# Kernel tuning notes

Measured on AMD Instinct MI355X. Metric: run time of the kernel, lower is better.

## Reference

```python
import jax, jax.numpy as jnp
import numpy as np

B, N, ENC, DEC, ATT = 32, 4096, 1024, 512, 512


def setup_inputs() -> dict:
    key = jax.random.key(0)
    ks = jax.random.split(key, 8)
    s_enc = 1.0 / np.sqrt(ENC)
    s_dec = 1.0 / np.sqrt(DEC)
    s_att = 1.0 / np.sqrt(ATT)
    return {
        "encoder_out": jax.random.normal(ks[0], (B, N, ENC), jnp.float32),
        "decoder_hidden": jax.random.normal(ks[1], (B, DEC), jnp.float32),
        "W_enc": jax.random.uniform(ks[2], (ENC, ATT), jnp.float32, -s_enc, s_enc),
        "b_enc": jax.random.uniform(ks[3], (ATT,), jnp.float32, -s_enc, s_enc),
        "W_dec": jax.random.uniform(ks[4], (DEC, ATT), jnp.float32, -s_dec, s_dec),
        "b_dec": jax.random.uniform(ks[5], (ATT,), jnp.float32, -s_dec, s_dec),
        "w_full": jax.random.uniform(ks[6], (ATT,), jnp.float32, -s_att, s_att),
        "b_full": jax.random.uniform(ks[7], (), jnp.float32, -s_att, s_att),
    }


def reference(encoder_out, decoder_hidden, W_enc, b_enc, W_dec, b_dec, w_full, b_full):
    # att1: [B, N, ATT]; att2: [B, 1, ATT]
    att1 = jnp.einsum('bne,ea->bna', encoder_out, W_enc) + b_enc
    att2 = (decoder_hidden @ W_dec + b_dec)[:, None, :]
    att = jax.nn.relu(att1 + att2)
    e = jnp.einsum('bna,a->bn', att, w_full) + b_full  # [B, N]
    alpha = jax.nn.softmax(e, axis=1)
    awe = jnp.einsum('bne,bn->be', encoder_out, alpha)  # weighted encoding [B, ENC]
    return awe, alpha
```

## Files before the change

### kernel.cpp

```cpp
#include <hip/hip_runtime.h>

#define B_ 32
#define N_ 4096
#define ENC_ 1024
#define DEC_ 512
#define ATT_ 512

typedef __attribute__((ext_vector_type(8))) short short8;
typedef __attribute__((ext_vector_type(4))) float f32x4;

__device__ __forceinline__ short f2bf(float f) {
  union { float f; unsigned u; } x; x.f = f;
  unsigned r = (x.u + 0x7FFFu + ((x.u >> 16) & 1u)) >> 16;
  return (short)r;
}

__device__ __forceinline__ void gl_lds16(const void* g, void* l) {
  __builtin_amdgcn_global_load_lds(
      (const __attribute__((address_space(1))) unsigned int*)g,
      (__attribute__((address_space(3))) unsigned int*)l, 16, 0, 0);
}

extern "C" __global__ void __launch_bounds__(256) prep_kernel(
    const float* __restrict__ dh, const float* __restrict__ W_dec,
    const float* __restrict__ b_dec, const float* __restrict__ b_enc,
    const float* __restrict__ W_enc,
    float* __restrict__ att2, short* __restrict__ Wfrag)
{
  if (blockIdx.x < B_) {
    __shared__ float dhs[DEC_];
    int b = blockIdx.x;
    for (int i = threadIdx.x; i < DEC_; i += 256) dhs[i] = dh[b * DEC_ + i];
    __syncthreads();
    for (int a = threadIdx.x; a < ATT_; a += 256) {
      float s = b_dec[a] + b_enc[a];
      for (int k = 0; k < DEC_; ++k) s += dhs[k] * W_dec[k * ATT_ + a];
      att2[b * ATT_ + a] = s;
    }
  } else {
    int idx = (blockIdx.x - B_) * 256 + threadIdx.x;
    int l = idx & 63;
    int t = (idx >> 6) & 31;
    int c = idx >> 11;
    int col = c * 16 + (l & 15);
    int kb = t * 32 + (l >> 4) * 8;
    short8 p;
#pragma unroll
    for (int j = 0; j < 8; ++j) p[j] = f2bf(W_enc[(kb + j) * ATT_ + col]);
    *(short8*)(Wfrag + ((long)idx << 3)) = p;
  }
}

extern "C" __global__ void __launch_bounds__(512, 2) gemm_e_kernel(
    const float* __restrict__ enc, const short* __restrict__ Wfrag,
    const float* __restrict__ att2, const float* __restrict__ w_full,
    float* __restrict__ e_out)
{
  __shared__ __align__(16) short As[2][128 * 32];
  __shared__ __align__(16) short Bs[2][32 * 512];
  __shared__ float e_red[2][64][4];

  const int tid = threadIdx.x;
  const int lane = tid & 63;
  const int w = tid >> 6;
  const int wr = w >> 2;
  const int wc = w & 3;
  const int blk = blockIdx.x;
  const int b = blk >> 5;
  const int n0 = (blk & 31) * 128;

  const int arow = tid >> 2;
  const int akc = tid & 3;
  const float* aptr = enc + ((long)(blk * 128 + arow)) * ENC_ + akc * 8;
  const int awbyte = (arow * 64 + akc * 16) ^ ((arow & 7) << 4);

  int arbyte[4];
#pragma unroll
  for (int r = 0; r < 4; ++r) {
    int rr = wr * 64 + r * 16 + (lane & 15);
    arbyte[r] = (rr * 64 + ((lane >> 4) * 16)) ^ ((rr & 7) << 4);
  }

  f32x4 acc[4][8] = {};

#pragma unroll
  for (int jj = 0; jj < 4; ++jj) {
    int c = (w << 2) + jj;
    gl_lds16(Wfrag + (((long)(c * 32 + 0) * 64 + lane) << 3), &Bs[0][c << 9]);
  }
  {
    f32x4 a0 = *(const f32x4*)(aptr);
    f32x4 a1 = *(const f32x4*)(aptr + 4);
    short8 p;
#pragma unroll
    for (int j = 0; j < 4; ++j) { p[j] = f2bf(a0[j]); p[j + 4] = f2bf(a1[j]); }
    *(short8*)((char*)(&As[0][0]) + awbyte) = p;
  }
  __syncthreads();

  for (int t = 0; t < 32; ++t) {
    const int cur = t & 1, nxt = cur ^ 1;
    f32x4 a0, a1;
    if (t < 31) {
#pragma unroll
      for (int jj = 0; jj < 4; ++jj) {
        int c = (w << 2) + jj;
        gl_lds16(Wfrag + (((long)(c * 32 + (t + 1)) * 64 + lane) << 3),
                 &Bs[nxt][c << 9]);
      }
      a0 = *(const f32x4*)(aptr + (t + 1) * 32);
      a1 = *(const f32x4*)(aptr + (t + 1) * 32 + 4);
    }

    short8 af[4];
#pragma unroll
    for (int r = 0; r < 4; ++r)
      af[r] = *(const short8*)((const char*)(&As[cur][0]) + arbyte[r]);
#pragma unroll
    for (int cc = 0; cc < 8; ++cc) {
      short8 bfg = *(const short8*)(&Bs[cur][((wc * 8 + cc) << 9) + (lane << 3)]);
#pragma unroll
      for (int r = 0; r < 4; ++r)
        acc[r][cc] = __builtin_amdgcn_mfma_f32_16x16x32_bf16(af[r], bfg,
                                                             acc[r][cc], 0, 0, 0);
    }

    if (t < 31) {
      short8 p;
#pragma unroll
      for (int j = 0; j < 4; ++j) { p[j] = f2bf(a0[j]); p[j + 4] = f2bf(a1[j]); }
      *(short8*)((char*)(&As[nxt][0]) + awbyte) = p;
    }
    __syncthreads();
  }

  const int lq = lane >> 4, lr = lane & 15;
  float at2v[8], wv[8];
#pragma unroll
  for (int cc = 0; cc < 8; ++cc) {
    int col = wc * 128 + cc * 16 + lr;
    at2v[cc] = att2[b * ATT_ + col];
    wv[cc] = w_full[col];
  }
#pragma unroll
  for (int r = 0; r < 4; ++r) {
#pragma unroll
    for (int j = 0; j < 4; ++j) {
      float s = 0.f;
#pragma unroll
      for (int cc = 0; cc < 8; ++cc)
        s += fmaxf(acc[r][cc][j] + at2v[cc], 0.f) * wv[cc];
      s += __shfl_xor(s, 1); s += __shfl_xor(s, 2);
      s += __shfl_xor(s, 4); s += __shfl_xor(s, 8);
      if (lr == 0) e_red[wr][r * 16 + lq * 4 + j][wc] = s;
    }
  }
  __syncthreads();
  if (tid < 128) {
    int wrr = tid >> 6, rl = tid & 63;
    float ev = e_red[wrr][rl][0] + e_red[wrr][rl][1] +
               e_red[wrr][rl][2] + e_red[wrr][rl][3];
    e_out[b * N_ + n0 + wrr * 64 + rl] = ev;
  }
}

extern "C" __global__ void __launch_bounds__(256) softmax_kernel(
    const float* __restrict__ e, float* __restrict__ alpha)
{
  int b = blockIdx.x, tid = threadIdx.x;
  float v[16];
  float m = -1e30f;
#pragma unroll
  for (int i = 0; i < 16; ++i) {
    v[i] = e[b * N_ + i * 256 + tid];
    m = fmaxf(m, v[i]);
  }
  for (int off = 1; off < 64; off <<= 1) m = fmaxf(m, __shfl_xor(m, off));
  __shared__ float redm[4];
  if ((tid & 63) == 0) redm[tid >> 6] = m;
  __syncthreads();
  m = fmaxf(fmaxf(redm[0], redm[1]), fmaxf(redm[2], redm[3]));
  float s = 0.f;
#pragma unroll
  for (int i = 0; i < 16; ++i) { v[i] = expf(v[i] - m); s += v[i]; }
  for (int off = 1; off < 64; off <<= 1) s += __shfl_xor(s, off);
  __shared__ float reds[4];
  if ((tid & 63) == 0) reds[tid >> 6] = s;
  __syncthreads();
  s = reds[0] + reds[1] + reds[2] + reds[3];
  float inv = 1.0f / s;
#pragma unroll
  for (int i = 0; i < 16; ++i) alpha[b * N_ + i * 256 + tid] = v[i] * inv;
}

extern "C" __global__ void __launch_bounds__(256) awe_part_kernel(
    const float* __restrict__ enc, const float* __restrict__ alpha,
    float* __restrict__ part)
{
  __shared__ float als[256];
  __shared__ f32x4 red[256];
  int bi = blockIdx.x;
  int b = bi & 31, cchunk = (bi >> 5) & 3, nchunk = bi >> 7;
  int t = threadIdx.x;
  int n0 = nchunk * 256;
  als[t] = alpha[b * N_ + n0 + t];
  __syncthreads();
  int tcol = t & 63, tn = t >> 6;
  const float* base = enc + (long)b * N_ * ENC_ + (long)n0 * ENC_ +
                      cchunk * 256 + tcol * 4;
  f32x4 acc = {};
  for (int i = tn; i < 256; i += 4) {
    f32x4 vv = *(const f32x4*)(base + (long)i * ENC_);
    acc += als[i] * vv;
  }
  red[t] = acc;
  __syncthreads();
  if (t < 64) {
    f32x4 s = red[t] + red[t + 64] + red[t + 128] + red[t + 192];
    *(f32x4*)(&part[(long)nchunk * 32768 + b * 1024 + cchunk * 256 + t * 4]) = s;
  }
}

extern "C" __global__ void __launch_bounds__(256) awe_reduce_kernel(
    const float* __restrict__ part, float* __restrict__ awe)
{
  int i = blockIdx.x * 256 + threadIdx.x;
  float s = 0.f;
#pragma unroll
  for (int p = 0; p < 16; ++p) s += part[(long)p * 32768 + i];
  awe[i] = s;
}

extern "C" void kernel_launch(void* const* d_in, const int* in_sizes, int n_in,
                              void* d_out, int out_size, void* d_ws, size_t ws_size,
                              hipStream_t stream) {
  const float* enc    = (const float*)d_in[0];
  const float* dh     = (const float*)d_in[1];
  const float* W_enc  = (const float*)d_in[2];
  const float* b_enc  = (const float*)d_in[3];
  const float* W_dec  = (const float*)d_in[4];
  const float* b_dec  = (const float*)d_in[5];
  const float* w_full = (const float*)d_in[6];
  float* out = (float*)d_out;

  char* ws = (char*)d_ws;
  float* att2  = (float*)ws;
  short* Wfrag = (short*)(ws + 65536);
  float* e_buf = (float*)(ws + 65536 + 1048576);
  float* part  = (float*)(ws + 65536 + 1048576 + 524288);

  hipLaunchKernelGGL(prep_kernel, dim3(B_ + 256), dim3(256), 0, stream,
                     dh, W_dec, b_dec, b_enc, W_enc, att2, Wfrag);
  hipLaunchKernelGGL(gemm_e_kernel, dim3(1024), dim3(512), 0, stream,
                     enc, Wfrag, att2, w_full, e_buf);
  hipLaunchKernelGGL(softmax_kernel, dim3(B_), dim3(256), 0, stream,
                     e_buf, out + B_ * ENC_);
  hipLaunchKernelGGL(awe_part_kernel, dim3(2048), dim3(256), 0, stream,
                     enc, out + B_ * ENC_, part);
  hipLaunchKernelGGL(awe_reduce_kernel, dim3(128), dim3(256), 0, stream,
                     part, out);
}
```

Before: 373.4 us.

## Shrink GEMM tile to 64 rows, load W fragments directly from global

The GEMM+score kernel moves from 128-row to 64-row tiles, doubling the grid to 2048 blocks. Each of the 8 waves now owns 64 attention columns and reads its bf16 W fragments straight from global/L2 into registers, so the large LDS buffer for B is dropped. LDS drops to a small double-buffered A tile, launch bounds allow 4 blocks per CU, and A prefetch now runs two steps ahead. The aim is higher occupancy and less LDS traffic, at the cost of more redundant W reads through L2 and per-iteration global-load latency on the MFMA path.

New measurement: 331.8 us. -11.1%, faster.

```diff
diff --git a/kernel.cpp b/kernel.cpp
--- a/kernel.cpp
+++ b/kernel.cpp
@@ -7,6 +7,7 @@
 #define ATT_ 512
 
 typedef __attribute__((ext_vector_type(8))) short short8;
+typedef __attribute__((ext_vector_type(4))) short short4v;
 typedef __attribute__((ext_vector_type(4))) float f32x4;
 
 __device__ __forceinline__ short f2bf(float f) {
@@ -15,10 +16,10 @@
   return (short)r;
 }
 
-__device__ __forceinline__ void gl_lds16(const void* g, void* l) {
-  __builtin_amdgcn_global_load_lds(
-      (const __attribute__((address_space(1))) unsigned int*)g,
-      (__attribute__((address_space(3))) unsigned int*)l, 16, 0, 0);
+__device__ __forceinline__ void lds_barrier() {
+  asm volatile("s_waitcnt lgkmcnt(0)" ::: "memory");
+  __builtin_amdgcn_s_barrier();
+  asm volatile("" ::: "memory");
 }
 
 extern "C" __global__ void __launch_bounds__(256) prep_kernel(
@@ -51,96 +52,87 @@
   }
 }
 
-extern "C" __global__ void __launch_bounds__(512, 2) gemm_e_kernel(
+extern "C" __global__ void __launch_bounds__(512, 4) gemm_e_kernel(
     const float* __restrict__ enc, const short* __restrict__ Wfrag,
     const float* __restrict__ att2, const float* __restrict__ w_full,
     float* __restrict__ e_out)
 {
-  __shared__ __align__(16) short As[2][128 * 32];
-  __shared__ __align__(16) short Bs[2][32 * 512];
-  __shared__ float e_red[2][64][4];
+  __shared__ __align__(16) short As[2][64 * 32];
+  __shared__ float e_red[64][8];
 
   const int tid = threadIdx.x;
   const int lane = tid & 63;
   const int w = tid >> 6;
-  const int wr = w >> 2;
-  const int wc = w & 3;
   const int blk = blockIdx.x;
-  const int b = blk >> 5;
-  const int n0 = (blk & 31) * 128;
-
-  const int arow = tid >> 2;
-  const int akc = tid & 3;
-  const float* aptr = enc + ((long)(blk * 128 + arow)) * ENC_ + akc * 8;
-  const int awbyte = (arow * 64 + akc * 16) ^ ((arow & 7) << 4);
+  const int b = blk >> 6;
+  const int n0 = (blk & 63) * 64;
+
+  const int arow = tid >> 3;
+  const int akc = tid & 7;
+  const float* aptr = enc + ((long)(b * N_ + n0 + arow)) * ENC_ + akc * 4;
+  const int awbyte = (arow * 64 + akc * 8) ^ ((arow & 7) << 4);
 
   int arbyte[4];
 #pragma unroll
   for (int r = 0; r < 4; ++r) {
-    int rr = wr * 64 + r * 16 + (lane & 15);
+    int rr = r * 16 + (lane & 15);
     arbyte[r] = (rr * 64 + ((lane >> 4) * 16)) ^ ((rr & 7) << 4);
   }
 
-  f32x4 acc[4][8] = {};
-
-#pragma unroll
-  for (int jj = 0; jj < 4; ++jj) {
-    int c = (w << 2) + jj;
-    gl_lds16(Wfrag + (((long)(c * 32 + 0) * 64 + lane) << 3), &Bs[0][c << 9]);
-  }
+  const short* bbase = Wfrag + (long)(w * 4) * 32 * 512 + lane * 8;
+
+  f32x4 acc[4][4] = {};
+
   {
-    f32x4 a0 = *(const f32x4*)(aptr);
-    f32x4 a1 = *(const f32x4*)(aptr + 4);
-    short8 p;
-#pragma unroll
-    for (int j = 0; j < 4; ++j) { p[j] = f2bf(a0[j]); p[j + 4] = f2bf(a1[j]); }
-    *(short8*)((char*)(&As[0][0]) + awbyte) = p;
-  }
-  __syncthreads();
-
+    f32x4 p0 = *(const f32x4*)(aptr);
+    short4v q;
+#pragma unroll
+    for (int j = 0; j < 4; ++j) q[j] = f2bf(p0[j]);
+    *(short4v*)((char*)(&As[0][0]) + awbyte) = q;
+  }
+  f32x4 pA = *(const f32x4*)(aptr + 32);
+  lds_barrier();
+
+#pragma unroll 2
   for (int t = 0; t < 32; ++t) {
-    const int cur = t & 1, nxt = cur ^ 1;
-    f32x4 a0, a1;
-    if (t < 31) {
-#pragma unroll
-      for (int jj = 0; jj < 4; ++jj) {
-        int c = (w << 2) + jj;
-        gl_lds16(Wfrag + (((long)(c * 32 + (t + 1)) * 64 + lane) << 3),
-                 &Bs[nxt][c << 9]);
-      }
-      a0 = *(const f32x4*)(aptr + (t + 1) * 32);
-      a1 = *(const f32x4*)(aptr + (t + 1) * 32 + 4);
-    }
+    const int cur = t & 1;
+    f32x4 pB;
+    if (t + 2 < 32) pB = *(const f32x4*)(aptr + (t + 2) * 32);
+
+    short8 bfg[4];
+#pragma unroll
+    for (int c = 0; c < 4; ++c)
+      bfg[c] = *(const short8*)(bbase + c * 16384 + t * 512);
 
     short8 af[4];
 #pragma unroll
     for (int r = 0; r < 4; ++r)
       af[r] = *(const short8*)((const char*)(&As[cur][0]) + arbyte[r]);
-#pragma unroll
-    for (int cc = 0; cc < 8; ++cc) {
-      short8 bfg = *(const short8*)(&Bs[cur][((wc * 8 + cc) << 9) + (lane << 3)]);
+
+#pragma unroll
+    for (int c = 0; c < 4; ++c)
 #pragma unroll
       for (int r = 0; r < 4; ++r)
-        acc[r][cc] = __builtin_amdgcn_mfma_f32_16x16x32_bf16(af[r], bfg,
-                                                             acc[r][cc], 0, 0, 0);
+        acc[r][c] = __builtin_amdgcn_mfma_f32_16x16x32_bf16(af[r], bfg[c],
+                                                            acc[r][c], 0, 0, 0);
+
+    if (t + 1 < 32) {
+      short4v q;
+#pragma unroll
+      for (int j = 0; j < 4; ++j) q[j] = f2bf(pA[j]);
+      *(short4v*)((char*)(&As[cur ^ 1][0]) + awbyte) = q;
     }
-
-    if (t < 31) {
-      short8 p;
-#pragma unroll
-      for (int j = 0; j < 4; ++j) { p[j] = f2bf(a0[j]); p[j + 4] = f2bf(a1[j]); }
-      *(short8*)((char*)(&As[nxt][0]) + awbyte) = p;
-    }
-    __syncthreads();
+    pA = pB;
+    lds_barrier();
   }
 
   const int lq = lane >> 4, lr = lane & 15;
-  float at2v[8], wv[8];
-#pragma unroll
-  for (int cc = 0; cc < 8; ++cc) {
-    int col = wc * 128 + cc * 16 + lr;
-    at2v[cc] = att2[b * ATT_ + col];
-    wv[cc] = w_full[col];
+  float at2v[4], wv[4];
+#pragma unroll
+  for (int c = 0; c < 4; ++c) {
+    int col = w * 64 + c * 16 + lr;
+    at2v[c] = att2[b * ATT_ + col];
+    wv[c] = w_full[col];
   }
 #pragma unroll
   for (int r = 0; r < 4; ++r) {
@@ -148,19 +140,19 @@
     for (int j = 0; j < 4; ++j) {
       float s = 0.f;
 #pragma unroll
-      for (int cc = 0; cc < 8; ++cc)
-        s += fmaxf(acc[r][cc][j] + at2v[cc], 0.f) * wv[cc];
+      for (int c = 0; c < 4; ++c)
+        s += fmaxf(acc[r][c][j] + at2v[c], 0.f) * wv[c];
       s += __shfl_xor(s, 1); s += __shfl_xor(s, 2);
       s += __shfl_xor(s, 4); s += __shfl_xor(s, 8);
-      if (lr == 0) e_red[wr][r * 16 + lq * 4 + j][wc] = s;
+      if (lr == 0) e_red[r * 16 + lq * 4 + j][w] = s;
     }
   }
   __syncthreads();
-  if (tid < 128) {
-    int wrr = tid >> 6, rl = tid & 63;
-    float ev = e_red[wrr][rl][0] + e_red[wrr][rl][1] +
-               e_red[wrr][rl][2] + e_red[wrr][rl][3];
-    e_out[b * N_ + n0 + wrr * 64 + rl] = ev;
+  if (tid < 64) {
+    float ev = 0.f;
+#pragma unroll
+    for (int ww = 0; ww < 8; ++ww) ev += e_red[tid][ww];
+    e_out[b * N_ + n0 + tid] = ev;
   }
 }
 
@@ -251,7 +243,7 @@
 
   hipLaunchKernelGGL(prep_kernel, dim3(B_ + 256), dim3(256), 0, stream,
                      dh, W_dec, b_dec, b_enc, W_enc, att2, Wfrag);
-  hipLaunchKernelGGL(gemm_e_kernel, dim3(1024), dim3(512), 0, stream,
+  hipLaunchKernelGGL(gemm_e_kernel, dim3(2048), dim3(512), 0, stream,
                      enc, Wfrag, att2, w_full, e_buf);
   hipLaunchKernelGGL(softmax_kernel, dim3(B_), dim3(256), 0, stream,
                      e_buf, out + B_ * ENC_);
```
